# Kernel optimization log

Measured on AMD Instinct MI355X. Metric: run time of the kernel, lower is better.

Reference implementation:

```python
import jax, jax.numpy as jnp
import numpy as np

EPS = 1e-10
LN_EPS = 1e-5
WIN = 64          # entropy_window_size
STRIDE = WIN // 2 # 32
CDF_POINTS = 64   # entropy_cdf_points
D_MODEL = 256
STATS_DIM = 256 + 1 + CDF_POINTS  # 321
HID = 2 * D_MODEL  # 512


def setup_inputs() -> dict:
    key = jax.random.key(0)
    ks = jax.random.split(key, 8)
    B, L = 64, 65536
    x = jax.random.randint(ks[0], (B, L), 0, 256)

    def lin(k, fan_in, fan_out):
        return jax.random.normal(k, (fan_in, fan_out), jnp.float32) * (1.0 / np.sqrt(fan_in))

    return {
        "x": x,
        "W1": lin(ks[1], STATS_DIM, HID), "b1": jnp.zeros((HID,), jnp.float32),
        "g1": jnp.ones((HID,), jnp.float32), "be1": jnp.zeros((HID,), jnp.float32),
        "W2": lin(ks[2], HID, HID), "b2": jnp.zeros((HID,), jnp.float32),
        "g2": jnp.ones((HID,), jnp.float32), "be2": jnp.zeros((HID,), jnp.float32),
        "W3": lin(ks[3], HID, D_MODEL), "b3": jnp.zeros((D_MODEL,), jnp.float32),
    }


def _entropy(counts):
    # Shannon entropy (bits) over last axis; matches torch compute_entropy.
    total = counts.sum(axis=-1, keepdims=True)
    probs = counts / (total + EPS)
    return -(probs * jnp.log2(probs + EPS)).sum(axis=-1)


def _layernorm(h, g, b):
    mu = h.mean(axis=-1, keepdims=True)
    var = ((h - mu) ** 2).mean(axis=-1, keepdims=True)
    return (h - mu) * jax.lax.rsqrt(var + LN_EPS) * g + b


def reference(x, W1, b1, g1, be1, W2, b2, g2, be2, W3, b3):
    B, L = x.shape
    xb = jnp.clip(x, 0, 255)

    # Global byte histogram via scatter-add (no one-hot materialization).
    hist = jnp.zeros((B, 256), jnp.float32).at[jnp.arange(B)[:, None], xb].add(1.0)
    normalized_hist = hist / (jnp.float32(L) + EPS)
    global_entropy = _entropy(hist)[:, None]  # [B,1]

    nw = (L - WIN) // STRIDE + 1
    widx = jnp.arange(nw)[:, None] * STRIDE + jnp.arange(WIN)[None, :]
    wins = xb[:, widx].reshape(B * nw, WIN)
    rows = jnp.arange(B * nw)[:, None]
    whist = jnp.zeros((B * nw, 256), jnp.float32).at[rows, wins].add(1.0)
    went = _entropy(whist).reshape(B, nw)  # [B, nw]

    # Empirical CDF of window entropies at linspace(0,8,CDF_POINTS).
    levels = jnp.linspace(0.0, 8.0, CDF_POINTS)
    cdf = (went[:, :, None] <= levels[None, None, :]).astype(jnp.float32).mean(axis=1)

    feats = jnp.concatenate([normalized_hist, global_entropy, cdf], axis=1)  # [B, 321]

    # Projector MLP (dropout omitted: eval mode).
    h = _layernorm(feats @ W1 + b1, g1, be1)
    h = jax.nn.relu(h)
    h = _layernorm(h @ W2 + b2, g2, be2)
    h = jax.nn.relu(h)
    return h @ W3 + b3  # [B, d_model]
```

## Files before the change

### kernel.cpp

```cpp
#include <hip/hip_runtime.h>

#define BATCH 64
#define LLEN 65536
#define NW 2047
#define STATS 321
#define NCHUNK 32

__device__ __forceinline__ float dppWaveSumBcast(float x) {
    float t;
    t = __int_as_float(__builtin_amdgcn_update_dpp(0, __float_as_int(x), 0x111, 0xf, 0xf, true));  x += t;
    t = __int_as_float(__builtin_amdgcn_update_dpp(0, __float_as_int(x), 0x112, 0xf, 0xf, true));  x += t;
    t = __int_as_float(__builtin_amdgcn_update_dpp(0, __float_as_int(x), 0x114, 0xf, 0xf, true));  x += t;
    t = __int_as_float(__builtin_amdgcn_update_dpp(0, __float_as_int(x), 0x118, 0xf, 0xf, true));  x += t;
    t = __int_as_float(__builtin_amdgcn_update_dpp(0, __float_as_int(x), 0x142, 0xa, 0xf, false)); x += t;
    t = __int_as_float(__builtin_amdgcn_update_dpp(0, __float_as_int(x), 0x143, 0xc, 0xf, false)); x += t;
    return __int_as_float(__builtin_amdgcn_readlane(__float_as_int(x), 63));
}

__global__ __launch_bounds__(256) void front_kernel(const int* __restrict__ x,
                                                    int* __restrict__ hpart,
                                                    int* __restrict__ cpart) {
    __shared__ int lh[256];
    __shared__ int lc[256];
    const int row = blockIdx.y;
    const int c = blockIdx.x;
    const int t = threadIdx.x;
    lh[t] = 0;
    __syncthreads();

    const int base = row * LLEN + c * 2048;
#pragma unroll
    for (int it = 0; it < 8; ++it) {
        int v = x[base + it * 256 + t];
        atomicAdd(&lh[min(max(v, 0), 255)], 1);
    }

    const int lane = t & 63;
    const int wave = t >> 6;
    const float lv = (lane == 63) ? 8.0f : (float)lane * (8.0f / 63.0f);
    const float T = (6.0f - lv) * 64.0f;
    const int wbase = c * 64 + wave * 16;

    int vv[16];
#pragma unroll
    for (int i = 0; i < 16; ++i) {
        const int w = min(wbase + i, NW - 1);
        vv[i] = x[row * LLEN + (w << 5) + lane];
    }
    int cnt = 0;
#pragma unroll
    for (int i = 0; i < 16; ++i) {
        const int v = vv[i];
        unsigned long long m = ~0ull;
#pragma unroll
        for (int k = 0; k < 8; ++k) {
            const unsigned long long b = __ballot(v & (1 << k));
            m &= ((v >> k) & 1) ? b : ~b;
        }
        const float S = dppWaveSumBcast(__log2f((float)__popcll(m)));
        cnt += (int)((S >= T) && (wbase + i < NW));
    }
    lc[t] = cnt;
    __syncthreads();

    hpart[(row * NCHUNK + c) * 256 + t] = lh[t];
    if (t < 64)
        cpart[(row * NCHUNK + c) * 64 + t] = lc[t] + lc[64 + t] + lc[128 + t] + lc[192 + t];
}

__global__ __launch_bounds__(256) void gemm1_kernel(
    const int* __restrict__ hpart, const int* __restrict__ cpart,
    const float* __restrict__ W, const float* __restrict__ b,
    float* __restrict__ out) {
    __shared__ float sa[STATS];
    __shared__ float red[4];
    __shared__ float part[16][64];
    const int row = blockIdx.y;
    const int t = threadIdx.x;

    int h = 0;
    const int* hp = hpart + row * (NCHUNK * 256) + t;
#pragma unroll
    for (int ch = 0; ch < NCHUNK; ++ch) h += hp[ch * 256];
    const float p = (float)h * (1.0f / 65536.0f);
    sa[t] = p;
    const float term = -p * log2f(p + 1e-10f);
    const float s = dppWaveSumBcast(term);
    if ((t & 63) == 0) red[t >> 6] = s;

    if (t < 64) {
        int cc = 0;
        const int* cp = cpart + row * (NCHUNK * 64) + t;
#pragma unroll
        for (int ch = 0; ch < NCHUNK; ++ch) cc += cp[ch * 64];
        sa[257 + t] = (float)cc * (1.0f / 2047.0f);
    }
    __syncthreads();
    if (t == 0) sa[256] = red[0] + red[1] + red[2] + red[3];
    __syncthreads();

    const int cl = (t & 15) * 4;
    const int col = blockIdx.x * 64 + cl;
    const int kg = t >> 4;
    const int klo = kg * 21;
    const int khi = min(klo + 21, STATS);
    float4 acc = {0.f, 0.f, 0.f, 0.f};
    for (int k = klo; k < khi; ++k) {
        const float a = sa[k];
        const float4 w = *(const float4*)&W[k * 512 + col];
        acc.x = fmaf(a, w.x, acc.x);
        acc.y = fmaf(a, w.y, acc.y);
        acc.z = fmaf(a, w.z, acc.z);
        acc.w = fmaf(a, w.w, acc.w);
    }
    *(float4*)&part[kg][cl] = acc;
    __syncthreads();
    if (t < 64) {
        float o = b[blockIdx.x * 64 + t];
#pragma unroll
        for (int g = 0; g < 16; ++g) o += part[g][t];
        out[row * 512 + blockIdx.x * 64 + t] = o;
    }
}

template <int NOUT, int CPB>
__global__ __launch_bounds__(256) void gemm_ln_kernel(
    const float* __restrict__ raw, const float* __restrict__ g,
    const float* __restrict__ be, const float* __restrict__ W,
    const float* __restrict__ b, float* __restrict__ out) {
    constexpr int TC = CPB / 4;
    constexpr int KG = 256 / TC;
    constexpr int KI = 512 / KG;
    __shared__ float sa[512];
    __shared__ float red[8];
    __shared__ float part[KG][CPB];
    const int row = blockIdx.y;
    const int t = threadIdx.x;

    const float v1 = raw[row * 512 + t];
    const float v2 = raw[row * 512 + 256 + t];
    const float s = dppWaveSumBcast(v1 + v2);
    const float q = dppWaveSumBcast(v1 * v1 + v2 * v2);
    if ((t & 63) == 0) { red[t >> 6] = s; red[4 + (t >> 6)] = q; }
    __syncthreads();
    const float mu = (red[0] + red[1] + red[2] + red[3]) * (1.0f / 512.0f);
    const float var = (red[4] + red[5] + red[6] + red[7]) * (1.0f / 512.0f) - mu * mu;
    const float rs = rsqrtf(var + 1e-5f);
    sa[t] = fmaxf((v1 - mu) * rs * g[t] + be[t], 0.0f);
    sa[t + 256] = fmaxf((v2 - mu) * rs * g[t + 256] + be[t + 256], 0.0f);
    __syncthreads();

    const int cl = (t % TC) * 4;
    const int col = blockIdx.x * CPB + cl;
    const int kg = t / TC;
    float4 acc = {0.f, 0.f, 0.f, 0.f};
#pragma unroll
    for (int i = 0; i < KI; ++i) {
        const int k = kg * KI + i;
        const float a = sa[k];
        const float4 w = *(const float4*)&W[k * NOUT + col];
        acc.x = fmaf(a, w.x, acc.x);
        acc.y = fmaf(a, w.y, acc.y);
        acc.z = fmaf(a, w.z, acc.z);
        acc.w = fmaf(a, w.w, acc.w);
    }
    *(float4*)&part[kg][cl] = acc;
    __syncthreads();
    if (t < CPB) {
        float o = b[blockIdx.x * CPB + t];
#pragma unroll
        for (int gi = 0; gi < KG; ++gi) o += part[gi][t];
        out[row * NOUT + blockIdx.x * CPB + t] = o;
    }
}

extern "C" void kernel_launch(void* const* d_in, const int* in_sizes, int n_in,
                              void* d_out, int out_size, void* d_ws, size_t ws_size,
                              hipStream_t stream) {
    const int* x = (const int*)d_in[0];
    const float* W1 = (const float*)d_in[1];
    const float* b1 = (const float*)d_in[2];
    const float* g1 = (const float*)d_in[3];
    const float* be1 = (const float*)d_in[4];
    const float* W2 = (const float*)d_in[5];
    const float* b2 = (const float*)d_in[6];
    const float* g2 = (const float*)d_in[7];
    const float* be2 = (const float*)d_in[8];
    const float* W3 = (const float*)d_in[9];
    const float* b3 = (const float*)d_in[10];
    float* out = (float*)d_out;

    char* ws = (char*)d_ws;
    int* hpart = (int*)ws;
    int* cpart = (int*)(ws + 2097152);
    float* raw1 = (float*)(ws + 2621440);
    float* raw2 = (float*)(ws + 2752512);

    front_kernel<<<dim3(NCHUNK, BATCH), 256, 0, stream>>>(x, hpart, cpart);
    gemm1_kernel<<<dim3(8, BATCH), 256, 0, stream>>>(hpart, cpart, W1, b1, raw1);
    gemm_ln_kernel<512, 64><<<dim3(8, BATCH), 256, 0, stream>>>(raw1, g1, be1, W2, b2, raw2);
    gemm_ln_kernel<256, 32><<<dim3(8, BATCH), 256, 0, stream>>>(raw2, g2, be2, W3, b3, out);
}
```

Baseline: 119.6 us.

## Fuse MLP stages into one kernel with per-row spin barriers; stage input in LDS

The three MLP kernels become one launch. The 8 blocks of each row synchronise between layers through global atomic counters that the front kernel resets. The front kernel now loads its chunk once with int4 loads into shared memory, plus a 64-int halo. It builds both the histogram and the windowed entropy counts from that LDS copy instead of re-reading global memory per window. This removes two kernel launches and the redundant global reads. In exchange it relies on all 8 blocks of a row being co-resident, otherwise the spin barriers can deadlock.

```diff
diff --git a/kernel.cpp b/kernel.cpp
--- a/kernel.cpp
+++ b/kernel.cpp
@@ -17,40 +17,61 @@
     return __int_as_float(__builtin_amdgcn_readlane(__float_as_int(x), 63));
 }
 
+__device__ __forceinline__ void rowBarrier(int* ctr) {
+    __syncthreads();
+    if (threadIdx.x == 0) {
+        __threadfence();
+        atomicAdd(ctr, 1);
+        while (atomicAdd(ctr, 0) < 8) __builtin_amdgcn_s_sleep(2);
+        __threadfence();
+    }
+    __syncthreads();
+}
+
 __global__ __launch_bounds__(256) void front_kernel(const int* __restrict__ x,
                                                     int* __restrict__ hpart,
-                                                    int* __restrict__ cpart) {
+                                                    int* __restrict__ cpart,
+                                                    int* __restrict__ bar) {
+    __shared__ __align__(16) int ls[2112];
     __shared__ int lh[256];
     __shared__ int lc[256];
     const int row = blockIdx.y;
     const int c = blockIdx.x;
     const int t = threadIdx.x;
     lh[t] = 0;
-    __syncthreads();
-
-    const int base = row * LLEN + c * 2048;
-#pragma unroll
-    for (int it = 0; it < 8; ++it) {
-        int v = x[base + it * 256 + t];
-        atomicAdd(&lh[min(max(v, 0), 255)], 1);
-    }
+    if (c == 0 && t < 2) bar[t * 64 + row] = 0;
+    __syncthreads();
+
+    const int base4 = (row * LLEN + c * 2048) >> 2;
+    const int4* xv = (const int4*)x;
+    const int4 a0 = xv[base4 + t];
+    const int4 a1 = xv[base4 + 256 + t];
+    ((int4*)ls)[t] = a0;
+    ((int4*)ls)[256 + t] = a1;
+    if (t < 16) {
+        const int gi = min(base4 + 512 + t, (BATCH * LLEN) / 4 - 1);
+        ((int4*)ls)[512 + t] = xv[gi];
+    }
+    atomicAdd(&lh[min(max(a0.x, 0), 255)], 1);
+    atomicAdd(&lh[min(max(a0.y, 0), 255)], 1);
+    atomicAdd(&lh[min(max(a0.z, 0), 255)], 1);
+    atomicAdd(&lh[min(max(a0.w, 0), 255)], 1);
+    atomicAdd(&lh[min(max(a1.x, 0), 255)], 1);
+    atomicAdd(&lh[min(max(a1.y, 0), 255)], 1);
+    atomicAdd(&lh[min(max(a1.z, 0), 255)], 1);
+    atomicAdd(&lh[min(max(a1.w, 0), 255)], 1);
+    __syncthreads();
 
     const int lane = t & 63;
     const int wave = t >> 6;
     const float lv = (lane == 63) ? 8.0f : (float)lane * (8.0f / 63.0f);
     const float T = (6.0f - lv) * 64.0f;
     const int wbase = c * 64 + wave * 16;
-
-    int vv[16];
+    const int lbase = wave * 512 + lane;
+    int cnt = 0;
 #pragma unroll
     for (int i = 0; i < 16; ++i) {
-        const int w = min(wbase + i, NW - 1);
-        vv[i] = x[row * LLEN + (w << 5) + lane];
-    }
-    int cnt = 0;
-#pragma unroll
-    for (int i = 0; i < 16; ++i) {
-        const int v = vv[i];
+        const int v = min(max(ls[lbase + i * 32], 0), 255);
         unsigned long long m = ~0ull;
 #pragma unroll
         for (int k = 0; k < 8; ++k) {
@@ -68,14 +89,20 @@
         cpart[(row * NCHUNK + c) * 64 + t] = lc[t] + lc[64 + t] + lc[128 + t] + lc[192 + t];
 }
 
-__global__ __launch_bounds__(256) void gemm1_kernel(
+__global__ __launch_bounds__(256) void mlp_kernel(
     const int* __restrict__ hpart, const int* __restrict__ cpart,
-    const float* __restrict__ W, const float* __restrict__ b,
-    float* __restrict__ out) {
-    __shared__ float sa[STATS];
-    __shared__ float red[4];
-    __shared__ float part[16][64];
+    const float* __restrict__ W1, const float* __restrict__ b1,
+    const float* __restrict__ g1, const float* __restrict__ be1,
+    const float* __restrict__ W2, const float* __restrict__ b2,
+    const float* __restrict__ g2, const float* __restrict__ be2,
+    const float* __restrict__ W3, const float* __restrict__ b3,
+    float* __restrict__ raw1, float* __restrict__ raw2,
+    int* __restrict__ bar, float* __restrict__ out) {
+    __shared__ float sa[512];
+    __shared__ float part[1024];
+    __shared__ float red[8];
     const int row = blockIdx.y;
+    const int cx = blockIdx.x;
     const int t = threadIdx.x;
 
     int h = 0;
@@ -87,7 +114,6 @@
     const float term = -p * log2f(p + 1e-10f);
     const float s = dppWaveSumBcast(term);
     if ((t & 63) == 0) red[t >> 6] = s;
-
     if (t < 64) {
         int cc = 0;
         const int* cp = cpart + row * (NCHUNK * 64) + t;
@@ -99,78 +125,107 @@
     if (t == 0) sa[256] = red[0] + red[1] + red[2] + red[3];
     __syncthreads();
 
-    const int cl = (t & 15) * 4;
-    const int col = blockIdx.x * 64 + cl;
-    const int kg = t >> 4;
-    const int klo = kg * 21;
-    const int khi = min(klo + 21, STATS);
-    float4 acc = {0.f, 0.f, 0.f, 0.f};
-    for (int k = klo; k < khi; ++k) {
-        const float a = sa[k];
-        const float4 w = *(const float4*)&W[k * 512 + col];
-        acc.x = fmaf(a, w.x, acc.x);
-        acc.y = fmaf(a, w.y, acc.y);
-        acc.z = fmaf(a, w.z, acc.z);
-        acc.w = fmaf(a, w.w, acc.w);
-    }
-    *(float4*)&part[kg][cl] = acc;
+    {
+        const int cl = (t & 15) * 4;
+        const int col = cx * 64 + cl;
+        const int kg = t >> 4;
+        const int klo = kg * 21;
+        const int khi = min(klo + 21, STATS);
+        float4 acc = {0.f, 0.f, 0.f, 0.f};
+        for (int k = klo; k < khi; ++k) {
+            const float a = sa[k];
+            const float4 w = *(const float4*)&W1[k * 512 + col];
+            acc.x = fmaf(a, w.x, acc.x);
+            acc.y = fmaf(a, w.y, acc.y);
+            acc.z = fmaf(a, w.z, acc.z);
+            acc.w = fmaf(a, w.w, acc.w);
+        }
+        *(float4*)&part[kg * 64 + cl] = acc;
+    }
     __syncthreads();
     if (t < 64) {
-        float o = b[blockIdx.x * 64 + t];
-#pragma unroll
-        for (int g = 0; g < 16; ++g) o += part[g][t];
-        out[row * 512 + blockIdx.x * 64 + t] = o;
-    }
-}
-
-template <int NOUT, int CPB>
-__global__ __launch_bounds__(256) void gemm_ln_kernel(
-    const float* __restrict__ raw, const float* __restrict__ g,
-    const float* __restrict__ be, const float* __restrict__ W,
-    const float* __restrict__ b, float* __restrict__ out) {
-    constexpr int TC = CPB / 4;
-    constexpr int KG = 256 / TC;
-    constexpr int KI = 512 / KG;
-    __shared__ float sa[512];
-    __shared__ float red[8];
-    __shared__ float part[KG][CPB];
-    const int row = blockIdx.y;
-    const int t = threadIdx.x;
-
-    const float v1 = raw[row * 512 + t];
-    const float v2 = raw[row * 512 + 256 + t];
-    const float s = dppWaveSumBcast(v1 + v2);
-    const float q = dppWaveSumBcast(v1 * v1 + v2 * v2);
-    if ((t & 63) == 0) { red[t >> 6] = s; red[4 + (t >> 6)] = q; }
-    __syncthreads();
-    const float mu = (red[0] + red[1] + red[2] + red[3]) * (1.0f / 512.0f);
-    const float var = (red[4] + red[5] + red[6] + red[7]) * (1.0f / 512.0f) - mu * mu;
-    const float rs = rsqrtf(var + 1e-5f);
-    sa[t] = fmaxf((v1 - mu) * rs * g[t] + be[t], 0.0f);
-    sa[t + 256] = fmaxf((v2 - mu) * rs * g[t + 256] + be[t + 256], 0.0f);
-    __syncthreads();
-
-    const int cl = (t % TC) * 4;
-    const int col = blockIdx.x * CPB + cl;
-    const int kg = t / TC;
-    float4 acc = {0.f, 0.f, 0.f, 0.f};
-#pragma unroll
-    for (int i = 0; i < KI; ++i) {
-        const int k = kg * KI + i;
-        const float a = sa[k];
-        const float4 w = *(const float4*)&W[k * NOUT + col];
-        acc.x = fmaf(a, w.x, acc.x);
-        acc.y = fmaf(a, w.y, acc.y);
-        acc.z = fmaf(a, w.z, acc.z);
-        acc.w = fmaf(a, w.w, acc.w);
-    }
-    *(float4*)&part[kg][cl] = acc;
-    __syncthreads();
-    if (t < CPB) {
-        float o = b[blockIdx.x * CPB + t];
-#pragma unroll
-        for (int gi = 0; gi < KG; ++gi) o += part[gi][t];
-        out[row * NOUT + blockIdx.x * CPB + t] = o;
+        float o = b1[cx * 64 + t];
+#pragma unroll
+        for (int g = 0; g < 16; ++g) o += part[g * 64 + t];
+        raw1[row * 512 + cx * 64 + t] = o;
+    }
+
+    rowBarrier(&bar[row]);
+
+    {
+        const float v1 = raw1[row * 512 + t];
+        const float v2 = raw1[row * 512 + 256 + t];
+        const float sm = dppWaveSumBcast(v1 + v2);
+        const float q = dppWaveSumBcast(v1 * v1 + v2 * v2);
+        if ((t & 63) == 0) { red[t >> 6] = sm; red[4 + (t >> 6)] = q; }
+        __syncthreads();
+        const float mu = (red[0] + red[1] + red[2] + red[3]) * (1.0f / 512.0f);
+        const float var = (red[4] + red[5] + red[6] + red[7]) * (1.0f / 512.0f) - mu * mu;
+        const float rs = rsqrtf(var + 1e-5f);
+        sa[t] = fmaxf((v1 - mu) * rs * g1[t] + be1[t], 0.0f);
+        sa[t + 256] = fmaxf((v2 - mu) * rs * g1[t + 256] + be1[t + 256], 0.0f);
+        __syncthreads();
+        const int cl = (t & 15) * 4;
+        const int col = cx * 64 + cl;
+        const int kg = t >> 4;
+        float4 acc = {0.f, 0.f, 0.f, 0.f};
+#pragma unroll
+        for (int i = 0; i < 32; ++i) {
+            const int k = kg * 32 + i;
+            const float a = sa[k];
+            const float4 w = *(const float4*)&W2[k * 512 + col];
+            acc.x = fmaf(a, w.x, acc.x);
+            acc.y = fmaf(a, w.y, acc.y);
+            acc.z = fmaf(a, w.z, acc.z);
+            acc.w = fmaf(a, w.w, acc.w);
+        }
+        *(float4*)&part[kg * 64 + cl] = acc;
+        __syncthreads();
+        if (t < 64) {
+            float o = b2[cx * 64 + t];
+#pragma unroll
+            for (int g = 0; g < 16; ++g) o += part[g * 64 + t];
+            raw2[row * 512 + cx * 64 + t] = o;
+        }
+    }
+
+    rowBarrier(&bar[64 + row]);
+
+    {
+        const float v1 = raw2[row * 512 + t];
+        const float v2 = raw2[row * 512 + 256 + t];
+        const float sm = dppWaveSumBcast(v1 + v2);
+        const float q = dppWaveSumBcast(v1 * v1 + v2 * v2);
+        if ((t & 63) == 0) { red[t >> 6] = sm; red[4 + (t >> 6)] = q; }
+        __syncthreads();
+        const float mu = (red[0] + red[1] + red[2] + red[3]) * (1.0f / 512.0f);
+        const float var = (red[4] + red[5] + red[6] + red[7]) * (1.0f / 512.0f) - mu * mu;
+        const float rs = rsqrtf(var + 1e-5f);
+        sa[t] = fmaxf((v1 - mu) * rs * g2[t] + be2[t], 0.0f);
+        sa[t + 256] = fmaxf((v2 - mu) * rs * g2[t + 256] + be2[t + 256], 0.0f);
+        __syncthreads();
+        const int cl = (t & 7) * 4;
+        const int col = cx * 32 + cl;
+        const int kg = t >> 3;
+        float4 acc = {0.f, 0.f, 0.f, 0.f};
+#pragma unroll
+        for (int i = 0; i < 16; ++i) {
+            const int k = kg * 16 + i;
+            const float a = sa[k];
+            const float4 w = *(const float4*)&W3[k * 256 + col];
+            acc.x = fmaf(a, w.x, acc.x);
+            acc.y = fmaf(a, w.y, acc.y);
+            acc.z = fmaf(a, w.z, acc.z);
+            acc.w = fmaf(a, w.w, acc.w);
+        }
+        *(float4*)&part[kg * 32 + cl] = acc;
+        __syncthreads();
+        if (t < 32) {
+            float o = b3[cx * 32 + t];
+#pragma unroll
+            for (int g = 0; g < 32; ++g) o += part[g * 32 + t];
+            out[row * 256 + cx * 32 + t] = o;
+        }
     }
 }
 
@@ -195,9 +250,10 @@
     int* cpart = (int*)(ws + 2097152);
     float* raw1 = (float*)(ws + 2621440);
     float* raw2 = (float*)(ws + 2752512);
-
-    front_kernel<<<dim3(NCHUNK, BATCH), 256, 0, stream>>>(x, hpart, cpart);
-    gemm1_kernel<<<dim3(8, BATCH), 256, 0, stream>>>(hpart, cpart, W1, b1, raw1);
-    gemm_ln_kernel<512, 64><<<dim3(8, BATCH), 256, 0, stream>>>(raw1, g1, be1, W2, b2, raw2);
-    gemm_ln_kernel<256, 32><<<dim3(8, BATCH), 256, 0, stream>>>(raw2, g2, be2, W3, b3, out);
-}
+    int* bar = (int*)(ws + 2883584);
+
+    front_kernel<<<dim3(NCHUNK, BATCH), 256, 0, stream>>>(x, hpart, cpart, bar);
+    mlp_kernel<<<dim3(8, BATCH), 256, 0, stream>>>(hpart, cpart, W1, b1, g1, be1,
+                                                   W2, b2, g2, be2, W3, b3,
+                                                   raw1, raw2, bar, out);
+}
```

After: 182.9 us. 53.0% more time.
